# Performance work log

Measured on AMD Instinct MI355X. Metric: run time of the kernel, lower is better.

Reference implementation:

```python
import jax, jax.numpy as jnp
import numpy as np

BN_EPS = 1e-5

def _conv1x1(x, w, b):
    # x: [B,C,H,W], w: [O,C], b: [O]
    return jnp.einsum('bchw,oc->bohw', x, w) + b[None, :, None, None]

def _maxpool2x2(x):
    B, C, H, W = x.shape
    return x.reshape(B, C, H // 2, 2, W // 2, 2).max(axis=(3, 5))

def setup_inputs() -> dict:
    key = jax.random.key(0)
    ks = jax.random.split(key, 6)
    B, C, H, W = 8, 256, 64, 64
    Ci = C // 2  # inter_channels default
    x = jax.random.normal(ks[0], (B, C, H, W), jnp.float32)
    s = lambda k, sh: jax.random.normal(k, sh, jnp.float32) * 0.02
    return {
        'x': x,
        'w_g': s(ks[1], (Ci, C)), 'b_g': jnp.zeros((Ci,), jnp.float32),
        'w_theta': s(ks[2], (Ci, C)), 'b_theta': jnp.zeros((Ci,), jnp.float32),
        'w_phi': s(ks[3], (Ci, C)), 'b_phi': jnp.zeros((Ci,), jnp.float32),
        'w_w': s(ks[4], (C, Ci)), 'b_w': jnp.zeros((C,), jnp.float32),
        'bn_gamma': 1.0 + 0.1 * jax.random.normal(ks[5], (C,), jnp.float32),
        'bn_beta': jnp.zeros((C,), jnp.float32),
    }

def reference(x, w_g, b_g, w_theta, b_theta, w_phi, b_phi, w_w, b_w, bn_gamma, bn_beta):
    B, C, H, W = x.shape
    Ci = w_g.shape[0]
    # projections (sub_sample=True: maxpool 2x2 on g and phi)
    g_x = _maxpool2x2(_conv1x1(x, w_g, b_g)).reshape(B, Ci, -1)          # [B,Ci,M]
    g_x = g_x.transpose(0, 2, 1)                                          # [B,M,Ci]
    theta_x = _conv1x1(x, w_theta, b_theta).reshape(B, Ci, -1)            # [B,Ci,N]
    theta_x = theta_x.transpose(0, 2, 1)                                  # [B,N,Ci]
    phi_x = _maxpool2x2(_conv1x1(x, w_phi, b_phi)).reshape(B, Ci, -1)     # [B,Ci,M]
    # unscaled embedded-Gaussian attention (no 1/sqrt(d), as in source)
    f = jnp.einsum('bnc,bcm->bnm', theta_x, phi_x)                        # [B,N,M]
    f_div_C = jax.nn.softmax(f, axis=-1)
    y = jnp.einsum('bnm,bmc->bnc', f_div_C, g_x)                          # [B,N,Ci]
    y = y.transpose(0, 2, 1).reshape(B, Ci, H, W)
    # W: 1x1 conv + BatchNorm (training mode: batch statistics)
    wy = _conv1x1(y, w_w, b_w)                                            # [B,C,H,W]
    mean = wy.mean(axis=(0, 2, 3), keepdims=True)
    var = wy.var(axis=(0, 2, 3), keepdims=True)
    wy = (wy - mean) * jax.lax.rsqrt(var + BN_EPS)
    wy = wy * bn_gamma[None, :, None, None] + bn_beta[None, :, None, None]
    return wy + x
```

## Files before the change

### kernel.cpp

```cpp
#include <hip/hip_runtime.h>
#include <hip/hip_bf16.h>

#define NB 8
#define NC 256
#define NCI 128
#define NSP 4096
#define NM 1024

typedef float f32x4 __attribute__((ext_vector_type(4)));
typedef float f32x16 __attribute__((ext_vector_type(16)));
typedef short s16x8 __attribute__((ext_vector_type(8)));
typedef unsigned short u16;

#define OFF_XH  (0ull)
#define OFF_THT (33554432ull)
#define OFF_PHT (41943040ull)
#define OFF_GP  (44040192ull)
#define OFF_YH  (46137344ull)
#define OFF_YL  (54525952ull)
#define OFF_WY  (0ull)
#define OFF_WBH (62914560ull)
#define OFF_WBL (63111168ull)
#define OFF_WWH (63307776ull)
#define OFF_WWL (63373312ull)
#define OFF_S   (63438848ull)

#define GLL(src, dst) __builtin_amdgcn_global_load_lds( \
    (const __attribute__((address_space(1))) unsigned*)(src), \
    (__attribute__((address_space(3))) unsigned*)(dst), 16, 0, 0)

__device__ __forceinline__ u16 f2bf(float f) {
  union { __hip_bfloat16 h; u16 u; } v;
  v.h = __float2bfloat16(f);
  return v.u;
}
__device__ __forceinline__ float bf2f(u16 u) {
  union { unsigned u; float f; } v;
  v.u = (unsigned)u << 16;
  return v.f;
}
__device__ __forceinline__ u16 bfmax4(u16 a, u16 b, u16 c, u16 d) {
  float v = fmaxf(fmaxf(bf2f(a), bf2f(b)), fmaxf(bf2f(c), bf2f(d)));
  return f2bf(v);
}
__device__ __forceinline__ unsigned cvtpk(float lo, float hi) {
  unsigned r;
  asm volatile("v_cvt_pk_bf16_f32 %0, %1, %2" : "=v"(r) : "v"(lo), "v"(hi));
  return r;
}

__global__ void zero_stats(float* s) { s[threadIdx.x] = 0.f; }

__global__ __launch_bounds__(256) void wcvt(
    const float* __restrict__ wg, const float* __restrict__ wth,
    const float* __restrict__ wph, const float* __restrict__ ww,
    u16* __restrict__ wbh, u16* __restrict__ wbl,
    u16* __restrict__ wwh, u16* __restrict__ wwl)
{
  int idx = blockIdx.x * 256 + threadIdx.x;
  if (idx < 384 * 256) {
    int row = idx >> 8, k = idx & 255;
    float v = row < 128 ? wg[row * 256 + k]
            : row < 256 ? wth[(row - 128) * 256 + k]
                        : wph[(row - 256) * 256 + k];
    u16 h = f2bf(v);
    wbh[idx] = h;
    wbl[idx] = f2bf(v - bf2f(h));
  } else {
    int j = idx - 384 * 256;
    float v = ww[j];
    u16 h = f2bf(v);
    wwh[j] = h;
    wwl[j] = f2bf(v - bf2f(h));
  }
}

__global__ __launch_bounds__(256) void xt_cvt(const float* __restrict__ x,
                                              u16* __restrict__ xh)
{
  __shared__ float t[64 * 68];
  const int n0 = blockIdx.x << 6, c0 = blockIdx.y << 6, b = blockIdx.z;
  const int tid = threadIdx.x;
  const int cl = tid >> 4, n4 = (tid & 15) << 2;
#pragma unroll
  for (int it = 0; it < 4; ++it) {
    int c = it * 16 + cl;
    float4 v = *(const float4*)&x[((size_t)(b * NC + c0 + c)) * NSP + n0 + n4];
    *(float4*)&t[c * 68 + n4] = v;
  }
  __syncthreads();
#pragma unroll
  for (int it = 0; it < 2; ++it) {
    int task = it * 256 + tid;
    int n = task >> 3, cc = (task & 7) << 3;
    u16 oh[8];
#pragma unroll
    for (int i = 0; i < 8; ++i) oh[i] = f2bf(t[(cc + i) * 68 + n]);
    *(s16x8*)&xh[((size_t)(b * NSP + n0 + n)) * NC + c0 + cc] = *(s16x8*)oh;
  }
}

__global__ __launch_bounds__(512, 1) void proj_fused(
    const u16* __restrict__ xh,
    const u16* __restrict__ wbh, const u16* __restrict__ wbl,
    const float* __restrict__ bg, const float* __restrict__ bth,
    const float* __restrict__ bph,
    u16* __restrict__ thT, u16* __restrict__ phT, u16* __restrict__ gp)
{
  __shared__ char smem[116224];
  u16* xsh = (u16*)smem;
  u16* wsh = (u16*)(smem + 16384);
  u16* wsl = (u16*)(smem + 65536);
  u16* outl = (u16*)smem;
  float* bias = (float*)(smem + 114688);

  const int b = blockIdx.y, h2 = blockIdx.x;
  const int n0 = h2 << 7;
  const int tid = threadIdx.x;
  const int wave = tid >> 6, lane = tid & 63;
  const int lo16 = lane & 15, hi4 = lane >> 4;
  const int wr = wave >> 1, wc = wave & 1;
  const int obase = wr * 96, nbase = wc * 64;

  if (tid < 384)
    bias[tid] = tid < 128 ? bg[tid] : tid < 256 ? bth[tid - 128] : bph[tid - 256];

  f32x4 acc[6][4];
#pragma unroll
  for (int i = 0; i < 6; ++i)
#pragma unroll
    for (int j = 0; j < 4; ++j) acc[i][j] = (f32x4){0.f, 0.f, 0.f, 0.f};

  for (int step = 0; step < 4; ++step) {
    __syncthreads();
#pragma unroll
    for (int i = 0; i < 2; ++i) {
      int ci = i * 512 + tid;
      int n = ci >> 3, slot = ci & 7;
      size_t rowb = ((size_t)(b * NSP + n0 + n)) * 512 + step * 128 + ((slot ^ (n & 7)) << 4);
      GLL((const char*)xh + rowb, (char*)xsh + (size_t)(i * 512 + (tid & ~63)) * 16);
    }
#pragma unroll
    for (int i = 0; i < 6; ++i) {
      int ci = i * 512 + tid;
      int o = ci >> 3, slot = ci & 7;
      size_t rowb = (size_t)o * 512 + step * 128 + ((slot ^ (o & 7)) << 4);
      GLL((const char*)wbh + rowb, (char*)wsh + (size_t)(i * 512 + (tid & ~63)) * 16);
      GLL((const char*)wbl + rowb, (char*)wsl + (size_t)(i * 512 + (tid & ~63)) * 16);
    }
    __syncthreads();

#pragma unroll
    for (int kc = 0; kc < 2; ++kc) {
      const int sl = kc * 4 + hi4;
      s16x8 bfh[4];
#pragma unroll
      for (int fn = 0; fn < 4; ++fn) {
        int n = nbase + fn * 16 + lo16;
        bfh[fn] = *(const s16x8*)((const char*)xsh + (int)n * 128 + ((sl ^ (n & 7)) << 4));
      }
      __builtin_amdgcn_s_setprio(1);
#pragma unroll
      for (int fo = 0; fo < 6; ++fo) {
        int o = obase + fo * 16 + lo16;
        int off = (int)o * 128 + ((sl ^ (o & 7)) << 4);
        s16x8 afh = *(const s16x8*)((const char*)wsh + off);
        s16x8 afl = *(const s16x8*)((const char*)wsl + off);
#pragma unroll
        for (int fn = 0; fn < 4; ++fn) {
          acc[fo][fn] = __builtin_amdgcn_mfma_f32_16x16x32_bf16(afh, bfh[fn], acc[fo][fn], 0, 0, 0);
          acc[fo][fn] = __builtin_amdgcn_mfma_f32_16x16x32_bf16(afl, bfh[fn], acc[fo][fn], 0, 0, 0);
        }
      }
      __builtin_amdgcn_s_setprio(0);
    }
  }

  __syncthreads();
#pragma unroll
  for (int fo = 0; fo < 6; ++fo) {
    int orow = obase + fo * 16 + hi4 * 4;
    f32x4 bv = *(const f32x4*)&bias[orow];
#pragma unroll
    for (int fn = 0; fn < 4; ++fn) {
      int n = nbase + fn * 16 + lo16;
#pragma unroll
      for (int r = 0; r < 4; ++r)
        outl[(orow + r) * 137 + n] = f2bf(acc[fo][fn][r] + bv[r]);
    }
  }
  __syncthreads();

#pragma unroll
  for (int it = 0; it < 4; ++it) {
    int task = it * 512 + tid;
    int n = task >> 4, cc = (task & 15) << 3;
    u16 o[8];
#pragma unroll
    for (int i = 0; i < 8; ++i) o[i] = outl[(128 + cc + i) * 137 + n];
    *(s16x8*)&thT[((size_t)(b * NSP + n0 + n)) * NCI + cc] = *(s16x8*)o;
  }
  {
    int c = tid >> 2, wq = tid & 3;
    u16 o[8];
#pragma unroll
    for (int j = 0; j < 8; ++j) {
      int w2 = wq * 8 + j;
      o[j] = bfmax4(outl[c * 137 + 2 * w2], outl[c * 137 + 2 * w2 + 1],
                    outl[c * 137 + 64 + 2 * w2], outl[c * 137 + 64 + 2 * w2 + 1]);
    }
    *(s16x8*)&gp[((size_t)(b * NCI + c)) * NM + (h2 << 5) + wq * 8] = *(s16x8*)o;
  }
  {
    int w2 = tid >> 4, cc = (tid & 15) << 3;
    u16 o[8];
#pragma unroll
    for (int i = 0; i < 8; ++i) {
      int c = 256 + cc + i;
      o[i] = bfmax4(outl[c * 137 + 2 * w2], outl[c * 137 + 2 * w2 + 1],
                    outl[c * 137 + 64 + 2 * w2], outl[c * 137 + 64 + 2 * w2 + 1]);
    }
    *(s16x8*)&phT[((size_t)(b * NM + (h2 << 5) + w2)) * NCI + cc] = *(s16x8*)o;
  }
}

__global__ __launch_bounds__(512, 2) void attn_mfma(
    const u16* __restrict__ thT, const u16* __restrict__ phT,
    const u16* __restrict__ gP, u16* __restrict__ yh, u16* __restrict__ yl)
{
  __shared__ char smem[131072];

  const int b = blockIdx.y;
  const int n0 = blockIdx.x << 7;
  const int tid = threadIdx.x;
  const int wave = tid >> 6;
  const int qg = wave & 3;
  const int kh = wave >> 2;
  const int lane = tid & 63;
  const int l31 = lane & 31;
  const int hi1 = lane >> 5;
  const int qbase = n0 + (qg << 5);
  const int swl = (l31 & 7) << 4;

  s16x8 thb[8];
  {
    const u16* tr = &thT[((size_t)b * NSP + qbase + l31) * NCI + hi1 * 8];
#pragma unroll
    for (int kc = 0; kc < 8; ++kc) thb[kc] = *(const s16x8*)&tr[kc * 16];
  }

  f32x16 yacc[4];
#pragma unroll
  for (int ct = 0; ct < 4; ++ct) yacc[ct] = (f32x16)0.f;
  float m_i = -3e38f, l_i = 0.f;

  auto stage = [&](int s, int step) {
    char* base = smem + s * 65536;
    const int m0a = step << 6, m0b = (step + 8) << 6;
#pragma unroll
    for (int it = 0; it < 8; ++it) {
      const int rg = it >> 1;
      int r = ((it & 1) << 9) + tid;
      char* dst = base + rg * 16384 + (size_t)(((it & 1) << 9) + (tid & ~63)) * 16;
      if (rg == 0 || rg == 2) {
        int m0 = (rg == 0) ? m0a : m0b;
        int m = r >> 4, cb = (r & 15) << 4;
        const char* src = (const char*)phT + (((size_t)b * NM + m0 + m) << 8) + (cb ^ ((m & 7) << 4));
        GLL(src, dst);
      } else {
        int m0 = (rg == 1) ? m0a : m0b;
        int c = r >> 3, mb = (r & 7) << 4;
        const char* src = (const char*)gP + (((size_t)b * NCI + c) << 11) + m0 * 2 + (mb ^ ((c & 7) << 4));
        GLL(src, dst);
      }
    }
  };

  stage(0, 0);
  __syncthreads();
  int cur = 0;

  for (int step = 0; step < 8; ++step) {
    if (step < 7) stage(cur ^ 1, step + 1);
    const char* ph = smem + cur * 65536 + kh * 32768;
    const char* gg = ph + 16384;

    f32x16 s0 = (f32x16)0.f, s1 = (f32x16)0.f;
    __builtin_amdgcn_s_setprio(1);
#pragma unroll
    for (int kc = 0; kc < 8; ++kc) {
      int cofs = (kc * 32 + hi1 * 16);
      s16x8 a0 = *(const s16x8*)(ph + l31 * 256 + (cofs ^ swl));
      s16x8 a1 = *(const s16x8*)(ph + (32 + l31) * 256 + (cofs ^ swl));
      s0 = __builtin_amdgcn_mfma_f32_32x32x16_bf16(a0, thb[kc], s0, 0, 0, 0);
      s1 = __builtin_amdgcn_mfma_f32_32x32x16_bf16(a1, thb[kc], s1, 0, 0, 0);
    }
    __builtin_amdgcn_s_setprio(0);

    float pm = s0[0];
#pragma unroll
    for (int i = 1; i < 16; ++i) pm = fmaxf(pm, s0[i]);
#pragma unroll
    for (int i = 0; i < 16; ++i) pm = fmaxf(pm, s1[i]);
    pm = fmaxf(pm, __shfl_xor(pm, 32));
    float mn = fmaxf(m_i, pm);
    float sc = __expf(m_i - mn);
    float rs = 0.f;
#pragma unroll
    for (int i = 0; i < 16; ++i) { s0[i] = __expf(s0[i] - mn); rs += s0[i]; }
#pragma unroll
    for (int i = 0; i < 16; ++i) { s1[i] = __expf(s1[i] - mn); rs += s1[i]; }
    rs += __shfl_xor(rs, 32);
    l_i = l_i * sc + rs;
    m_i = mn;
#pragma unroll
    for (int ct = 0; ct < 4; ++ct)
#pragma unroll
      for (int i = 0; i < 16; ++i) yacc[ct][i] *= sc;

    s16x8 pb[4];
#pragma unroll
    for (int km = 0; km < 4; ++km) {
      int r0 = (km & 1) * 8;
      unsigned X0, X1, X2, X3;
      if (km < 2) {
        X0 = cvtpk(s0[r0 + 0], s0[r0 + 1]);
        X1 = cvtpk(s0[r0 + 2], s0[r0 + 3]);
        X2 = cvtpk(s0[r0 + 4], s0[r0 + 5]);
        X3 = cvtpk(s0[r0 + 6], s0[r0 + 7]);
      } else {
        X0 = cvtpk(s1[r0 + 0], s1[r0 + 1]);
        X1 = cvtpk(s1[r0 + 2], s1[r0 + 3]);
        X2 = cvtpk(s1[r0 + 4], s1[r0 + 5]);
        X3 = cvtpk(s1[r0 + 6], s1[r0 + 7]);
      }
      asm volatile("v_permlane32_swap_b32 %0, %1" : "+v"(X0), "+v"(X2));
      asm volatile("v_permlane32_swap_b32 %0, %1" : "+v"(X1), "+v"(X3));
      unsigned d[4] = {X0, X1, X2, X3};
      pb[km] = *(s16x8*)d;
    }

    __builtin_amdgcn_s_setprio(1);
#pragma unroll
    for (int ct = 0; ct < 4; ++ct) {
      const char* grow = gg + (ct * 32 + l31) * 128;
#pragma unroll
      for (int km = 0; km < 4; ++km) {
        s16x8 ga = *(const s16x8*)(grow + ((km * 32 + hi1 * 16) ^ swl));
        yacc[ct] = __builtin_amdgcn_mfma_f32_32x32x16_bf16(ga, pb[km], yacc[ct], 0, 0, 0);
      }
    }
    __builtin_amdgcn_s_setprio(0);

    __syncthreads();
    cur ^= 1;
  }

  float* yx = (float*)smem;
  float* ml = (float*)(smem + 65536);
  const int slot = (qg << 6) + lane;
  if (kh == 1) {
#pragma unroll
    for (int ct = 0; ct < 4; ++ct)
#pragma unroll
      for (int i4 = 0; i4 < 4; ++i4) {
        f32x4 v = {yacc[ct][i4 * 4 + 0], yacc[ct][i4 * 4 + 1],
                   yacc[ct][i4 * 4 + 2], yacc[ct][i4 * 4 + 3]};
        *(f32x4*)((char*)yx + (size_t)(((ct * 4 + i4) << 8) + slot) * 16) = v;
      }
    ml[slot * 2] = m_i;
    ml[slot * 2 + 1] = l_i;
  }
  __syncthreads();
  if (kh == 1) return;

  float m1 = ml[slot * 2], l1 = ml[slot * 2 + 1];
  float mm = fmaxf(m_i, m1);
  float sc0 = __expf(m_i - mm), sc1 = __expf(m1 - mm);
  float inv = 1.f / (l_i * sc0 + l1 * sc1);
  float a0 = sc0 * inv, a1 = sc1 * inv;
#pragma unroll
  for (int ct = 0; ct < 4; ++ct)
#pragma unroll
    for (int i4 = 0; i4 < 4; ++i4) {
      f32x4 v = *(const f32x4*)((const char*)yx + (size_t)(((ct * 4 + i4) << 8) + slot) * 16);
#pragma unroll
      for (int j = 0; j < 4; ++j)
        yacc[ct][i4 * 4 + j] = yacc[ct][i4 * 4 + j] * a0 + v[j] * a1;
    }

  u16* bounce = (u16*)(smem + 67584) + qg * 4224;
  const int qq = lane >> 1, c0 = (lane & 1) << 6;
#pragma unroll
  for (int pass = 0; pass < 2; ++pass) {
#pragma unroll
    for (int ct = 0; ct < 4; ++ct) {
#pragma unroll
      for (int rp = 0; rp < 8; ++rp) {
        int r = rp * 2;
        int c = ct * 32 + (r & 3) + 8 * (r >> 2) + 4 * hi1;
        float v0 = yacc[ct][r], v1 = yacc[ct][r + 1];
        u16 h0 = f2bf(v0), h1 = f2bf(v1);
        u16 w0 = h0, w1 = h1;
        if (pass) { w0 = f2bf(v0 - bf2f(h0)); w1 = f2bf(v1 - bf2f(h1)); }
        *(unsigned*)&bounce[l31 * 132 + c] = (unsigned)w0 | ((unsigned)w1 << 16);
      }
    }
    asm volatile("s_waitcnt lgkmcnt(0)" ::: "memory");
    u16* dst = pass ? yl : yh;
    size_t row = ((size_t)b * NSP + qbase + qq) * NCI + c0;
#pragma unroll
    for (int k = 0; k < 8; ++k)
      *(s16x8*)&dst[row + k * 8] = *(const s16x8*)&bounce[qq * 132 + c0 + k * 8];
    asm volatile("s_waitcnt lgkmcnt(0)" ::: "memory");
  }
}

__global__ __launch_bounds__(512, 1) void conv_w_mfma(
    const u16* __restrict__ yh, const u16* __restrict__ yl,
    const u16* __restrict__ wwh, const u16* __restrict__ wwl,
    const float* __restrict__ bw, float* __restrict__ wy,
    float* __restrict__ s1g, float* __restrict__ s2g)
{
  __shared__ char smem[102400];
  u16* wsh = (u16*)smem;
  u16* wsl = (u16*)(smem + 32768);
  u16* ysh = (u16*)(smem + 65536);
  u16* ysl = (u16*)(smem + 81920);
  float (*sums1)[256] = (float(*)[256])(smem + 98304);
  float (*sums2)[256] = (float(*)[256])(smem + 100352);

  const int b = blockIdx.y, n0 = blockIdx.x << 7;
  const int tid = threadIdx.x;
  const int wave = tid >> 6, lane = tid & 63;
  const int lo16 = lane & 15, hi4 = lane >> 4;
  const int wr = wave >> 1, wc = wave & 1;
  const int obase = wr * 64, nbase = wc * 64;

  f32x4 acc[4][4];
#pragma unroll
  for (int i = 0; i < 4; ++i)
#pragma unroll
    for (int j = 0; j < 4; ++j) acc[i][j] = (f32x4){0.f, 0.f, 0.f, 0.f};

  for (int step = 0; step < 2; ++step) {
    __syncthreads();
#pragma unroll
    for (int i = 0; i < 4; ++i) {
      int ci = i * 512 + tid;
      int o = ci >> 3, slot = ci & 7;
      size_t rowb = (size_t)o * 256 + step * 128 + ((slot ^ (o & 7)) << 4);
      GLL((const char*)wwh + rowb, (char*)wsh + (size_t)(i * 512 + (tid & ~63)) * 16);
      GLL((const char*)wwl + rowb, (char*)wsl + (size_t)(i * 512 + (tid & ~63)) * 16);
    }
#pragma unroll
    for (int i = 0; i < 2; ++i) {
      int ci = i * 512 + tid;
      int n = ci >> 3, slot = ci & 7;
      size_t rowb = ((size_t)(b * NSP + n0 + n)) * 256 + step * 128 + ((slot ^ (n & 7)) << 4);
      GLL((const char*)yh + rowb, (char*)ysh + (size_t)(i * 512 + (tid & ~63)) * 16);
      GLL((const char*)yl + rowb, (char*)ysl + (size_t)(i * 512 + (tid & ~63)) * 16);
    }
    __syncthreads();

#pragma unroll
    for (int kc = 0; kc < 2; ++kc) {
      const int sl = kc * 4 + hi4;
      s16x8 bfh[4], bfl[4];
#pragma unroll
      for (int fn = 0; fn < 4; ++fn) {
        int n = nbase + fn * 16 + lo16;
        int off = (int)n * 128 + ((sl ^ (n & 7)) << 4);
        bfh[fn] = *(const s16x8*)((const char*)ysh + off);
        bfl[fn] = *(const s16x8*)((const char*)ysl + off);
      }
      __builtin_amdgcn_s_setprio(1);
#pragma unroll
      for (int fo = 0; fo < 4; ++fo) {
        int o = obase + fo * 16 + lo16;
        int off = (int)o * 128 + ((sl ^ (o & 7)) << 4);
        s16x8 afh = *(const s16x8*)((const char*)wsh + off);
        s16x8 afl = *(const s16x8*)((const char*)wsl + off);
#pragma unroll
        for (int fn = 0; fn < 4; ++fn) {
          acc[fo][fn] = __builtin_amdgcn_mfma_f32_16x16x32_bf16(afh, bfh[fn], acc[fo][fn], 0, 0, 0);
          acc[fo][fn] = __builtin_amdgcn_mfma_f32_16x16x32_bf16(afh, bfl[fn], acc[fo][fn], 0, 0, 0);
          acc[fo][fn] = __builtin_amdgcn_mfma_f32_16x16x32_bf16(afl, bfh[fn], acc[fo][fn], 0, 0, 0);
        }
      }
      __builtin_amdgcn_s_setprio(0);
    }
  }

#pragma unroll
  for (int fo = 0; fo < 4; ++fo) {
    int orow = obase + fo * 16 + hi4 * 4;
    float bv[4];
#pragma unroll
    for (int r = 0; r < 4; ++r) bv[r] = bw[orow + r];
    float ss[4] = {0.f, 0.f, 0.f, 0.f}, sq[4] = {0.f, 0.f, 0.f, 0.f};
#pragma unroll
    for (int fn = 0; fn < 4; ++fn) {
      int col = n0 + nbase + fn * 16 + lo16;
#pragma unroll
      for (int r = 0; r < 4; ++r) {
        float v = acc[fo][fn][r] + bv[r];
        wy[((size_t)(b * NC) + orow + r) * NSP + col] = v;
        ss[r] += v;
        sq[r] += v * v;
      }
    }
#pragma unroll
    for (int r = 0; r < 4; ++r) {
#pragma unroll
      for (int d = 1; d < 16; d <<= 1) {
        ss[r] += __shfl_xor(ss[r], d);
        sq[r] += __shfl_xor(sq[r], d);
      }
    }
    if (lo16 == 0) {
#pragma unroll
      for (int r = 0; r < 4; ++r) {
        sums1[wc][orow + r] = ss[r];
        sums2[wc][orow + r] = sq[r];
      }
    }
  }
  __syncthreads();
  if (tid < 256) {
    atomicAdd(&s1g[tid], sums1[0][tid] + sums1[1][tid]);
    atomicAdd(&s2g[tid], sums2[0][tid] + sums2[1][tid]);
  }
}

__global__ __launch_bounds__(256) void bn_res4(
    const float* __restrict__ wy, const float* __restrict__ x,
    const float* __restrict__ s1, const float* __restrict__ s2,
    const float* __restrict__ gamma, const float* __restrict__ beta,
    float* __restrict__ out)
{
  int i4 = (blockIdx.x * 256 + threadIdx.x) << 2;
  int c = (i4 >> 12) & 255;
  const float cnt = 1.f / 32768.f;
  float mean = s1[c] * cnt;
  float var = s2[c] * cnt - mean * mean;
  float inv = rsqrtf(var + 1e-5f) * gamma[c];
  float bet = beta[c];
  float4 w = *(const float4*)&wy[i4];
  float4 xv = *(const float4*)&x[i4];
  float4 o;
  o.x = (w.x - mean) * inv + bet + xv.x;
  o.y = (w.y - mean) * inv + bet + xv.y;
  o.z = (w.z - mean) * inv + bet + xv.z;
  o.w = (w.w - mean) * inv + bet + xv.w;
  *(float4*)&out[i4] = o;
}

extern "C" void kernel_launch(void* const* d_in, const int* in_sizes, int n_in,
                              void* d_out, int out_size, void* d_ws, size_t ws_size,
                              hipStream_t stream) {
  const float* x    = (const float*)d_in[0];
  const float* w_g  = (const float*)d_in[1];
  const float* b_g  = (const float*)d_in[2];
  const float* w_th = (const float*)d_in[3];
  const float* b_th = (const float*)d_in[4];
  const float* w_ph = (const float*)d_in[5];
  const float* b_ph = (const float*)d_in[6];
  const float* w_w  = (const float*)d_in[7];
  const float* b_w  = (const float*)d_in[8];
  const float* gam  = (const float*)d_in[9];
  const float* bet  = (const float*)d_in[10];
  float* out = (float*)d_out;
  char* ws = (char*)d_ws;

  u16*   xh  = (u16*)(ws + OFF_XH);
  u16*   thT = (u16*)(ws + OFF_THT);
  u16*   phT = (u16*)(ws + OFF_PHT);
  u16*   gp  = (u16*)(ws + OFF_GP);
  u16*   yhb = (u16*)(ws + OFF_YH);
  u16*   ylb = (u16*)(ws + OFF_YL);
  float* wy  = (float*)(ws + OFF_WY);
  u16*   wbh = (u16*)(ws + OFF_WBH);
  u16*   wbl = (u16*)(ws + OFF_WBL);
  u16*   wwh = (u16*)(ws + OFF_WWH);
  u16*   wwl = (u16*)(ws + OFF_WWL);
  float* s1  = (float*)(ws + OFF_S);
  float* s2  = s1 + 256;

  wcvt<<<dim3(512), 256, 0, stream>>>(w_g, w_th, w_ph, w_w, wbh, wbl, wwh, wwl);
  zero_stats<<<dim3(1), 512, 0, stream>>>(s1);
  xt_cvt<<<dim3(64, 4, 8), 256, 0, stream>>>(x, xh);

  proj_fused<<<dim3(32, 8), 512, 0, stream>>>(xh, wbh, wbl, b_g, b_th, b_ph, thT, phT, gp);

  attn_mfma<<<dim3(32, 8), 512, 0, stream>>>(thT, phT, gp, yhb, ylb);

  conv_w_mfma<<<dim3(32, 8), 512, 0, stream>>>(yhb, ylb, wwh, wwl, b_w, wy, s1, s2);

  bn_res4<<<dim3(8192), 256, 0, stream>>>(wy, x, s1, s2, gam, bet, out);
}
```

Measured before the change: 105.3 us.

## Halve attention query tile and split output channels across waves for more blocks

The attention kernel now processes 64 queries per block instead of 128, launching 512 blocks instead of 256. Waves are split by query group, by output-channel half and by key half. Each step handles 32 keys per half instead of 64, over 16 steps, with LDS shrunk to 64 KB and launch bounds raised to allow more resident blocks per CU. The goal is better CU occupancy and load balance. The cost is that each wave recomputes the QK^T scores and softmax for its channel half, and there are more barriers and more staging iterations.

```diff
diff --git a/kernel.cpp b/kernel.cpp
--- a/kernel.cpp
+++ b/kernel.cpp
@@ -224,23 +224,25 @@
   }
 }
 
-__global__ __launch_bounds__(512, 2) void attn_mfma(
+__global__ __launch_bounds__(512, 4) void attn_mfma(
     const u16* __restrict__ thT, const u16* __restrict__ phT,
     const u16* __restrict__ gP, u16* __restrict__ yh, u16* __restrict__ yl)
 {
-  __shared__ char smem[131072];
+  __shared__ char smem[65536];
 
   const int b = blockIdx.y;
-  const int n0 = blockIdx.x << 7;
+  const int n0 = blockIdx.x << 6;
   const int tid = threadIdx.x;
   const int wave = tid >> 6;
-  const int qg = wave & 3;
+  const int qg = wave & 1;
+  const int ch = (wave >> 1) & 1;
   const int kh = wave >> 2;
   const int lane = tid & 63;
   const int l31 = lane & 31;
   const int hi1 = lane >> 5;
   const int qbase = n0 + (qg << 5);
   const int swl = (l31 & 7) << 4;
+  const int gsw = ((l31 >> 1) & 3) << 4;
 
   s16x8 thb[8];
   {
@@ -249,28 +251,26 @@
     for (int kc = 0; kc < 8; ++kc) thb[kc] = *(const s16x8*)&tr[kc * 16];
   }
 
-  f32x16 yacc[4];
-#pragma unroll
-  for (int ct = 0; ct < 4; ++ct) yacc[ct] = (f32x16)0.f;
+  f32x16 yacc[2];
+#pragma unroll
+  for (int j = 0; j < 2; ++j) yacc[j] = (f32x16)0.f;
   float m_i = -3e38f, l_i = 0.f;
 
   auto stage = [&](int s, int step) {
-    char* base = smem + s * 65536;
-    const int m0a = step << 6, m0b = (step + 8) << 6;
-#pragma unroll
-    for (int it = 0; it < 8; ++it) {
-      const int rg = it >> 1;
-      int r = ((it & 1) << 9) + tid;
-      char* dst = base + rg * 16384 + (size_t)(((it & 1) << 9) + (tid & ~63)) * 16;
-      if (rg == 0 || rg == 2) {
-        int m0 = (rg == 0) ? m0a : m0b;
-        int m = r >> 4, cb = (r & 15) << 4;
+    char* base = smem + s * 32768;
+#pragma unroll
+    for (int it = 0; it < 4; ++it) {
+      const int kr = it >> 1;
+      const int part = it & 1;
+      const int m0 = kr * 512 + step * 32;
+      char* dst = base + kr * 16384 + part * 8192 + (size_t)(tid & ~63) * 16;
+      if (part == 0) {
+        int m = tid >> 4, cb = (tid & 15) << 4;
         const char* src = (const char*)phT + (((size_t)b * NM + m0 + m) << 8) + (cb ^ ((m & 7) << 4));
         GLL(src, dst);
       } else {
-        int m0 = (rg == 1) ? m0a : m0b;
-        int c = r >> 3, mb = (r & 7) << 4;
-        const char* src = (const char*)gP + (((size_t)b * NCI + c) << 11) + m0 * 2 + (mb ^ ((c & 7) << 4));
+        int c = tid >> 2, mb = (tid & 3) << 4;
+        const char* src = (const char*)gP + (((size_t)b * NCI + c) << 11) + m0 * 2 + (mb ^ (((c >> 1) & 3) << 4));
         GLL(src, dst);
       }
     }
@@ -280,60 +280,45 @@
   __syncthreads();
   int cur = 0;
 
-  for (int step = 0; step < 8; ++step) {
-    if (step < 7) stage(cur ^ 1, step + 1);
-    const char* ph = smem + cur * 65536 + kh * 32768;
-    const char* gg = ph + 16384;
-
-    f32x16 s0 = (f32x16)0.f, s1 = (f32x16)0.f;
+  for (int step = 0; step < 16; ++step) {
+    if (step < 15) stage(cur ^ 1, step + 1);
+    const char* ph = smem + cur * 32768 + kh * 16384;
+    const char* gg = ph + 8192;
+
+    f32x16 s0 = (f32x16)0.f;
     __builtin_amdgcn_s_setprio(1);
 #pragma unroll
     for (int kc = 0; kc < 8; ++kc) {
-      int cofs = (kc * 32 + hi1 * 16);
-      s16x8 a0 = *(const s16x8*)(ph + l31 * 256 + (cofs ^ swl));
-      s16x8 a1 = *(const s16x8*)(ph + (32 + l31) * 256 + (cofs ^ swl));
+      s16x8 a0 = *(const s16x8*)(ph + l31 * 256 + ((kc * 32 + hi1 * 16) ^ swl));
       s0 = __builtin_amdgcn_mfma_f32_32x32x16_bf16(a0, thb[kc], s0, 0, 0, 0);
-      s1 = __builtin_amdgcn_mfma_f32_32x32x16_bf16(a1, thb[kc], s1, 0, 0, 0);
     }
     __builtin_amdgcn_s_setprio(0);
 
     float pm = s0[0];
 #pragma unroll
     for (int i = 1; i < 16; ++i) pm = fmaxf(pm, s0[i]);
-#pragma unroll
-    for (int i = 0; i < 16; ++i) pm = fmaxf(pm, s1[i]);
     pm = fmaxf(pm, __shfl_xor(pm, 32));
     float mn = fmaxf(m_i, pm);
     float sc = __expf(m_i - mn);
     float rs = 0.f;
 #pragma unroll
     for (int i = 0; i < 16; ++i) { s0[i] = __expf(s0[i] - mn); rs += s0[i]; }
-#pragma unroll
-    for (int i = 0; i < 16; ++i) { s1[i] = __expf(s1[i] - mn); rs += s1[i]; }
     rs += __shfl_xor(rs, 32);
     l_i = l_i * sc + rs;
     m_i = mn;
 #pragma unroll
-    for (int ct = 0; ct < 4; ++ct)
-#pragma unroll
-      for (int i = 0; i < 16; ++i) yacc[ct][i] *= sc;
-
-    s16x8 pb[4];
-#pragma unroll
-    for (int km = 0; km < 4; ++km) {
-      int r0 = (km & 1) * 8;
-      unsigned X0, X1, X2, X3;
-      if (km < 2) {
-        X0 = cvtpk(s0[r0 + 0], s0[r0 + 1]);
-        X1 = cvtpk(s0[r0 + 2], s0[r0 + 3]);
-        X2 = cvtpk(s0[r0 + 4], s0[r0 + 5]);
-        X3 = cvtpk(s0[r0 + 6], s0[r0 + 7]);
-      } else {
-        X0 = cvtpk(s1[r0 + 0], s1[r0 + 1]);
-        X1 = cvtpk(s1[r0 + 2], s1[r0 + 3]);
-        X2 = cvtpk(s1[r0 + 4], s1[r0 + 5]);
-        X3 = cvtpk(s1[r0 + 6], s1[r0 + 7]);
-      }
+    for (int j = 0; j < 2; ++j)
+#pragma unroll
+      for (int i = 0; i < 16; ++i) yacc[j][i] *= sc;
+
+    s16x8 pb[2];
+#pragma unroll
+    for (int km = 0; km < 2; ++km) {
+      int r0 = km * 8;
+      unsigned X0 = cvtpk(s0[r0 + 0], s0[r0 + 1]);
+      unsigned X1 = cvtpk(s0[r0 + 2], s0[r0 + 3]);
+      unsigned X2 = cvtpk(s0[r0 + 4], s0[r0 + 5]);
+      unsigned X3 = cvtpk(s0[r0 + 6], s0[r0 + 7]);
       asm volatile("v_permlane32_swap_b32 %0, %1" : "+v"(X0), "+v"(X2));
       asm volatile("v_permlane32_swap_b32 %0, %1" : "+v"(X1), "+v"(X3));
       unsigned d[4] = {X0, X1, X2, X3};
@@ -342,12 +327,12 @@
 
     __builtin_amdgcn_s_setprio(1);
 #pragma unroll
-    for (int ct = 0; ct < 4; ++ct) {
-      const char* grow = gg + (ct * 32 + l31) * 128;
-#pragma unroll
-      for (int km = 0; km < 4; ++km) {
-        s16x8 ga = *(const s16x8*)(grow + ((km * 32 + hi1 * 16) ^ swl));
-        yacc[ct] = __builtin_amdgcn_mfma_f32_32x32x16_bf16(ga, pb[km], yacc[ct], 0, 0, 0);
+    for (int j = 0; j < 2; ++j) {
+      const char* grow = gg + (ch * 64 + j * 32 + l31) * 64;
+#pragma unroll
+      for (int km = 0; km < 2; ++km) {
+        s16x8 ga = *(const s16x8*)(grow + ((km * 32 + hi1 * 16) ^ gsw));
+        yacc[j] = __builtin_amdgcn_mfma_f32_32x32x16_bf16(ga, pb[km], yacc[j], 0, 0, 0);
       }
     }
     __builtin_amdgcn_s_setprio(0);
@@ -356,62 +341,66 @@
     cur ^= 1;
   }
 
-  float* yx = (float*)smem;
-  float* ml = (float*)(smem + 65536);
-  const int slot = (qg << 6) + lane;
+  const int w2 = wave & 3;
+  float* yx = (float*)(smem + w2 * 8192);
+  float* ml = (float*)(smem + 32768 + w2 * 512);
   if (kh == 1) {
 #pragma unroll
-    for (int ct = 0; ct < 4; ++ct)
+    for (int j = 0; j < 2; ++j)
 #pragma unroll
       for (int i4 = 0; i4 < 4; ++i4) {
-        f32x4 v = {yacc[ct][i4 * 4 + 0], yacc[ct][i4 * 4 + 1],
-                   yacc[ct][i4 * 4 + 2], yacc[ct][i4 * 4 + 3]};
-        *(f32x4*)((char*)yx + (size_t)(((ct * 4 + i4) << 8) + slot) * 16) = v;
-      }
-    ml[slot * 2] = m_i;
-    ml[slot * 2 + 1] = l_i;
+        f32x4 v = {yacc[j][i4 * 4 + 0], yacc[j][i4 * 4 + 1],
+                   yacc[j][i4 * 4 + 2], yacc[j][i4 * 4 + 3]};
+        *(f32x4*)((char*)yx + (size_t)((j * 4 + i4) * 64 + lane) * 16) = v;
+      }
+    ml[lane * 2] = m_i;
+    ml[lane * 2 + 1] = l_i;
   }
   __syncthreads();
   if (kh == 1) return;
 
-  float m1 = ml[slot * 2], l1 = ml[slot * 2 + 1];
-  float mm = fmaxf(m_i, m1);
-  float sc0 = __expf(m_i - mm), sc1 = __expf(m1 - mm);
-  float inv = 1.f / (l_i * sc0 + l1 * sc1);
-  float a0 = sc0 * inv, a1 = sc1 * inv;
-#pragma unroll
-  for (int ct = 0; ct < 4; ++ct)
-#pragma unroll
-    for (int i4 = 0; i4 < 4; ++i4) {
-      f32x4 v = *(const f32x4*)((const char*)yx + (size_t)(((ct * 4 + i4) << 8) + slot) * 16);
-#pragma unroll
-      for (int j = 0; j < 4; ++j)
-        yacc[ct][i4 * 4 + j] = yacc[ct][i4 * 4 + j] * a0 + v[j] * a1;
-    }
-
-  u16* bounce = (u16*)(smem + 67584) + qg * 4224;
-  const int qq = lane >> 1, c0 = (lane & 1) << 6;
+  {
+    float m1 = ml[lane * 2], l1 = ml[lane * 2 + 1];
+    float mm = fmaxf(m_i, m1);
+    float sc0 = __expf(m_i - mm), sc1 = __expf(m1 - mm);
+    float inv = 1.f / (l_i * sc0 + l1 * sc1);
+    float a0 = sc0 * inv, a1 = sc1 * inv;
+#pragma unroll
+    for (int j = 0; j < 2; ++j)
+#pragma unroll
+      for (int i4 = 0; i4 < 4; ++i4) {
+        f32x4 v = *(const f32x4*)((const char*)yx + (size_t)((j * 4 + i4) * 64 + lane) * 16);
+#pragma unroll
+        for (int k = 0; k < 4; ++k)
+          yacc[j][i4 * 4 + k] = yacc[j][i4 * 4 + k] * a0 + v[k] * a1;
+      }
+  }
+
+  u16* bounce = (u16*)(smem + 36864) + w2 * 2304;
+  const int qq0 = lane >> 3, cb8 = (lane & 7) << 3;
 #pragma unroll
   for (int pass = 0; pass < 2; ++pass) {
 #pragma unroll
-    for (int ct = 0; ct < 4; ++ct) {
+    for (int j = 0; j < 2; ++j) {
 #pragma unroll
       for (int rp = 0; rp < 8; ++rp) {
         int r = rp * 2;
-        int c = ct * 32 + (r & 3) + 8 * (r >> 2) + 4 * hi1;
-        float v0 = yacc[ct][r], v1 = yacc[ct][r + 1];
+        int cl = j * 32 + (r & 3) + 8 * (r >> 2) + 4 * hi1;
+        float v0 = yacc[j][r], v1 = yacc[j][r + 1];
         u16 h0 = f2bf(v0), h1 = f2bf(v1);
         u16 w0 = h0, w1 = h1;
         if (pass) { w0 = f2bf(v0 - bf2f(h0)); w1 = f2bf(v1 - bf2f(h1)); }
-        *(unsigned*)&bounce[l31 * 132 + c] = (unsigned)w0 | ((unsigned)w1 << 16);
+        *(unsigned*)&bounce[l31 * 72 + cl] = (unsigned)w0 | ((unsigned)w1 << 16);
       }
     }
     asm volatile("s_waitcnt lgkmcnt(0)" ::: "memory");
     u16* dst = pass ? yl : yh;
-    size_t row = ((size_t)b * NSP + qbase + qq) * NCI + c0;
-#pragma unroll
-    for (int k = 0; k < 8; ++k)
-      *(s16x8*)&dst[row + k * 8] = *(const s16x8*)&bounce[qq * 132 + c0 + k * 8];
+    size_t base = ((size_t)b * NSP + qbase) * NCI + ch * 64 + cb8;
+#pragma unroll
+    for (int it = 0; it < 4; ++it) {
+      int row = qq0 + it * 8;
+      *(s16x8*)&dst[base + (size_t)row * NCI] = *(const s16x8*)&bounce[row * 72 + cb8];
+    }
     asm volatile("s_waitcnt lgkmcnt(0)" ::: "memory");
   }
 }
@@ -593,7 +582,7 @@
 
   proj_fused<<<dim3(32, 8), 512, 0, stream>>>(xh, wbh, wbl, b_g, b_th, b_ph, thT, phT, gp);
 
-  attn_mfma<<<dim3(32, 8), 512, 0, stream>>>(thT, phT, gp, yhb, ylb);
+  attn_mfma<<<dim3(64, 8), 512, 0, stream>>>(thT, phT, gp, yhb, ylb);
 
   conv_w_mfma<<<dim3(32, 8), 512, 0, stream>>>(yhb, ylb, wwh, wwl, b_w, wy, s1, s2);
 
```

Measured after the change: 113.0 us. 1.07x slower.
